# Performance work log

Measured on AMD Instinct MI355X. Metric: run time of the kernel, lower is better.

The kernel has to match this reference:

```python
import jax, jax.numpy as jnp
import numpy as np

EPS = 1e-5


def clin(xr, xi, Wr, Wi, br, bi):
    # complex linear layer: (xr + i xi) @ (Wr + i Wi) + (br + i bi)
    yr = xr @ Wr - xi @ Wi + br
    yi = xr @ Wi + xi @ Wr + bi
    return yr, yi


def setup_inputs() -> dict:
    key = jax.random.key(0)
    ks = jax.random.split(key, 16)
    B, N, DE, DV = 4, 256, 128, 64
    s_in = 1.0 / np.sqrt(DE)
    s_p = 1.0 / np.sqrt(DV)
    f32 = jnp.float32
    inp = {
        'Z_q': jax.random.normal(ks[0], (B, 2, N, DE), f32),
        'Z_k': jax.random.normal(ks[1], (B, 2, N, DE), f32),
        'Z_v': jax.random.normal(ks[2], (B, 2, N, DE), f32),
        't_measure_all': jnp.tile(jnp.arange(N + 1, dtype=f32) * 0.01, (B, 1)),
        'Wq_r': jax.random.normal(ks[3], (DE, DV), f32) * s_in,
        'Wq_i': jax.random.normal(ks[4], (DE, DV), f32) * s_in,
        'bq_r': jnp.zeros((DV,), f32), 'bq_i': jnp.zeros((DV,), f32),
        'Wk_r': jax.random.normal(ks[5], (DE, DV), f32) * s_in,
        'Wk_i': jax.random.normal(ks[6], (DE, DV), f32) * s_in,
        'bk_r': jnp.zeros((DV,), f32), 'bk_i': jnp.zeros((DV,), f32),
        'Wv_r': jax.random.normal(ks[7], (DE, DV), f32) * s_in,
        'Wv_i': jax.random.normal(ks[8], (DE, DV), f32) * s_in,
        'bv_r': jnp.zeros((DV,), f32), 'bv_i': jnp.zeros((DV,), f32),
        'Wp_r': jax.random.normal(ks[9], (DV, DE), f32) * s_p,
        'Wp_i': jax.random.normal(ks[10], (DV, DE), f32) * s_p,
        'bp_r': jnp.zeros((DE,), f32), 'bp_i': jnp.zeros((DE,), f32),
        'lambda1': jax.random.normal(ks[11], (2, DV // 2), f32),
        'lambda_Omega_sqrt': jax.random.normal(ks[12], (DV,), f32) / DV,
        'lambda_Gamma_sqrt': jax.random.normal(ks[13], (DV,), f32) / DV,
        'noise_floor': jnp.array(1.0, f32),
        'tau': jnp.array(1.0, f32),
        'nu': jnp.array(1.0, f32),
        'eta_param': jnp.zeros((DV,), f32),
    }
    return inp


def reference(Z_q, Z_k, Z_v, t_measure_all,
              Wq_r, Wq_i, bq_r, bq_i, Wk_r, Wk_i, bk_r, bk_i,
              Wv_r, Wv_i, bv_r, bv_i, Wp_r, Wp_i, bp_r, bp_i,
              lambda1, lambda_Omega_sqrt, lambda_Gamma_sqrt,
              noise_floor, tau, nu, eta_param):
    N = Z_q.shape[2]
    # complex projections (B, N, d)
    Qr, Qi = clin(Z_q[:, 0], Z_q[:, 1], Wq_r, Wq_i, bq_r, bq_i)
    Kr_, Ki_ = clin(Z_k[:, 0], Z_k[:, 1], Wk_r, Wk_i, bk_r, bk_i)
    Vr, Vi = clin(Z_v[:, 0], Z_v[:, 1], Wv_r, Wv_i, bv_r, bv_i)
    # state-transition eigenvalues: stable conjugate pairs
    re = jnp.concatenate([-lambda1[0] ** 2, -lambda1[0] ** 2])  # (d_v,), Re<=0
    im = jnp.concatenate([lambda1[1], -lambda1[1]])             # (d_v,)
    lam_Om = lambda_Omega_sqrt ** 2
    lam_Ga = lambda_Gamma_sqrt ** 2 + EPS
    # pairwise complex exponential kernel exp(lambda * (t_i - t_j))
    t = t_measure_all[0, :-1]                       # (N,)
    dt = t[:, None] - t[None, :]                    # (N, N)
    amp = jnp.exp(re[None, None, :] * dt[:, :, None])
    ph = im[None, None, :] * dt[:, :, None]
    Ker = amp * jnp.cos(ph)                          # (N, N, d_v)
    Kei = amp * jnp.sin(ph)
    # propagated value estimates Z_hat_ij = exp(lam dt_ij) * V_j
    Zhr = Ker[None] * Vr[:, None] - Kei[None] * Vi[:, None]  # (B, N, N, d_v)
    Zhi = Ker[None] * Vi[:, None] + Kei[None] * Vr[:, None]
    # residuals R_ij = Q_i - exp(lam dt_ij) * K_j
    Rr = Qr[:, :, None, :] - (Ker[None] * Kr_[:, None] - Kei[None] * Ki_[:, None])
    Ri = Qi[:, :, None, :] - (Ker[None] * Ki_[:, None] + Kei[None] * Kr_[:, None])
    # per-pair covariance (OU-process propagation of measurement + process noise)
    adt = jnp.abs(dt)[:, :, None]
    exp2 = jnp.exp(2.0 * re * adt)                   # (N, N, d_v)
    Vij = lam_Ga * exp2 + lam_Om * (exp2 - 1.0) / (2.0 * (re - EPS))
    # mahalanobis distance and attention scores
    mah = (Rr ** 2 + Ri ** 2) / (Vij[None] + lam_Ga)          # (B, N, N, d_v)
    dist_sum = jnp.abs(nu) * jnp.sum(mah, axis=3, keepdims=True)
    base = Vij[None] * (noise_floor + dist_sum + EPS)
    scores = -jnp.abs(tau) * jnp.log(base)
    mask = jnp.tril(jnp.ones((N, N), bool))
    scores = jnp.where(mask[None, :, :, None], scores, -jnp.inf)
    Qij = jax.nn.softmax(scores, axis=2)             # normalize over j
    m = mask[None, :, :, None].astype(Zhr.dtype)
    Zhr = Zhr * m
    Zhi = Zhi * m
    est_vr = jnp.einsum('bijd,bijd->bid', Qij, Zhr)
    est_vi = jnp.einsum('bijd,bijd->bid', Qij, Zhi)
    # gated residual mix (double sigmoid as in source)
    eta = jax.nn.sigmoid(eta_param)
    g = jax.nn.sigmoid(eta)
    elr = (1.0 - eta) * Vr + g * est_vr
    eli = (1.0 - eta) * Vi + g * est_vi
    # one-step-ahead prediction via matrix exponential exp(lambda * h)
    h = t[1] - t[0]
    ma = jnp.exp(re * h)
    mr, mi = ma * jnp.cos(im * h), ma * jnp.sin(im * h)
    ppr = mr * elr - mi * eli
    ppi = mr * eli + mi * elr
    outr, outi = clin(ppr, ppi, Wp_r, Wp_i, bp_r, bp_i)
    est_latent = jnp.stack([elr, eli], axis=1)       # (B, 2, N, d_v)
    out = jnp.stack([outr, outi], axis=1)            # (B, 2, N, d_e)
    Zhat = jnp.stack([Zhr, Zhi], axis=1)             # (B, 2, N, N, d_v)
    lambda_h = jnp.stack([re, im])                   # (2, d_v)
    return est_latent, out, Qij, Zhat, lambda_h
```

## Files before the change

### kernel.cpp

```cpp
#include <hip/hip_runtime.h>
#include <math.h>

#define B_ 4
#define N_ 256
#define DE_ 128
#define DV_ 64
#define EPS_ 1e-5f

typedef __attribute__((ext_vector_type(4))) float f32x4;

__device__ __forceinline__ f32x4 ld4(const float* p) { return *(const f32x4*)p; }
__device__ __forceinline__ void st4(float* p, f32x4 v) { *(f32x4*)p = v; }

#define OFF_ETA   0
#define OFF_G     64
#define OFF_MR    128
#define OFF_MI    192
#define OFF_KER   256
#define OFF_KEI   (OFF_KER + N_*DV_)
#define OFF_A     (OFF_KEI + N_*DV_)
#define OFF_INV   (OFF_A + N_*DV_)
#define OFF_QR    (OFF_INV + N_*DV_)
#define OFF_QI    (OFF_QR + B_*N_*DV_)
#define OFF_KR    (OFF_QI + B_*N_*DV_)
#define OFF_KI    (OFF_KR + B_*N_*DV_)
#define OFF_VR    (OFF_KI + B_*N_*DV_)
#define OFF_VI    (OFF_VR + B_*N_*DV_)

#define OUT_EL    0
#define OUT_OUT   (B_*2*N_*DV_)
#define OUT_QIJ   (OUT_OUT + B_*2*N_*DE_)
#define OUT_ZHAT  (OUT_QIJ + B_*N_*N_*DV_)
#define OUT_LAMH  (OUT_ZHAT + (size_t)B_*2*N_*N_*DV_)

__global__ __launch_bounds__(256) void k_pre(
    const float* __restrict__ Zq, const float* __restrict__ Zk, const float* __restrict__ Zv,
    const float* __restrict__ Wqr, const float* __restrict__ Wqi,
    const float* __restrict__ bqr, const float* __restrict__ bqi,
    const float* __restrict__ Wkr, const float* __restrict__ Wki,
    const float* __restrict__ bkr, const float* __restrict__ bki,
    const float* __restrict__ Wvr, const float* __restrict__ Wvi,
    const float* __restrict__ bvr, const float* __restrict__ bvi,
    const float* __restrict__ t,  const float* __restrict__ lam1,
    const float* __restrict__ lOm, const float* __restrict__ lGa,
    const float* __restrict__ eta_p, const float* __restrict__ tau_p,
    float* __restrict__ ws, float* __restrict__ out)
{
    const int tid = (int)threadIdx.x;

    if (blockIdx.x >= 1024) {
        const int idx = (int)blockIdx.x - 1024;
        const int w = tid >> 6;
        const int d = tid & 63;
        const int delta = idx * 4 + w;

        const float l0 = lam1[d & 31];
        const float re = -l0 * l0;
        const float im = (d < 32) ? lam1[32 + d] : -lam1[d];

        const float lo = lOm[d];
        const float lam_Om = lo * lo;
        const float lg_ = lGa[d];
        const float lam_Ga = lg_ * lg_ + EPS_;
        const float tau_a = fabsf(tau_p[0]);

        const float t0 = t[0];
        const float dt = t[delta] - t0;

        const float amp = expf(re * dt);
        const float ph  = im * dt;
        const int td = delta * DV_ + d;
        ws[OFF_KER + td] = amp * cosf(ph);
        ws[OFF_KEI + td] = amp * sinf(ph);

        const float e2  = expf(2.0f * re * dt);
        const float vij = lam_Ga * e2 + lam_Om * (e2 - 1.0f) / (2.0f * (re - EPS_));
        ws[OFF_A   + td] = expf(-tau_a * logf(vij));
        ws[OFF_INV + td] = 1.0f / (vij + lam_Ga);

        if (delta == 0) {
            const float eta = 1.0f / (1.0f + expf(-eta_p[d]));
            const float g   = 1.0f / (1.0f + expf(-eta));
            ws[OFF_ETA + d] = eta;
            ws[OFF_G   + d] = g;
            const float h  = t[1] - t0;
            const float ma = expf(re * h);
            ws[OFF_MR + d] = ma * cosf(im * h);
            ws[OFF_MI + d] = ma * sinf(im * h);
            out[OUT_LAMH + d]       = re;
            out[OUT_LAMH + DV_ + d] = im;
        }
        return;
    }

    const int row = (int)blockIdx.x;
    const int b = row >> 8, n = row & (N_ - 1);

    __shared__ float x[6][DE_];
    __shared__ float red[4][6][DV_];

    if (tid < DE_) {
        x[0][tid] = Zq[((size_t)(b*2+0)*N_ + n)*DE_ + tid];
        x[1][tid] = Zq[((size_t)(b*2+1)*N_ + n)*DE_ + tid];
        x[2][tid] = Zk[((size_t)(b*2+0)*N_ + n)*DE_ + tid];
        x[3][tid] = Zk[((size_t)(b*2+1)*N_ + n)*DE_ + tid];
        x[4][tid] = Zv[((size_t)(b*2+0)*N_ + n)*DE_ + tid];
        x[5][tid] = Zv[((size_t)(b*2+1)*N_ + n)*DE_ + tid];
    }
    __syncthreads();

    const int w = tid >> 6;
    const int d = tid & 63;
    float aqr = 0.f, aqi = 0.f, akr = 0.f, aki = 0.f, avr = 0.f, avi = 0.f;
    const int k0 = w * 32;
    #pragma unroll 4
    for (int kk = 0; kk < 32; ++kk) {
        const int k = k0 + kk;
        const float xqr = x[0][k], xqi = x[1][k];
        const float xkr = x[2][k], xki = x[3][k];
        const float xvr = x[4][k], xvi = x[5][k];
        float wr, wi;
        wr = Wqr[k*DV_ + d]; wi = Wqi[k*DV_ + d];
        aqr += xqr*wr - xqi*wi; aqi += xqr*wi + xqi*wr;
        wr = Wkr[k*DV_ + d]; wi = Wki[k*DV_ + d];
        akr += xkr*wr - xki*wi; aki += xkr*wi + xki*wr;
        wr = Wvr[k*DV_ + d]; wi = Wvi[k*DV_ + d];
        avr += xvr*wr - xvi*wi; avi += xvr*wi + xvi*wr;
    }
    red[w][0][d] = aqr; red[w][1][d] = aqi;
    red[w][2][d] = akr; red[w][3][d] = aki;
    red[w][4][d] = avr; red[w][5][d] = avi;
    __syncthreads();

    if (tid < DV_) {
        const int o = row * DV_ + tid;
        ws[OFF_QR + o] = red[0][0][tid]+red[1][0][tid]+red[2][0][tid]+red[3][0][tid] + bqr[tid];
        ws[OFF_QI + o] = red[0][1][tid]+red[1][1][tid]+red[2][1][tid]+red[3][1][tid] + bqi[tid];
        ws[OFF_KR + o] = red[0][2][tid]+red[1][2][tid]+red[2][2][tid]+red[3][2][tid] + bkr[tid];
        ws[OFF_KI + o] = red[0][3][tid]+red[1][3][tid]+red[2][3][tid]+red[3][3][tid] + bki[tid];
        ws[OFF_VR + o] = red[0][4][tid]+red[1][4][tid]+red[2][4][tid]+red[3][4][tid] + bvr[tid];
        ws[OFF_VI + o] = red[0][5][tid]+red[1][5][tid]+red[2][5][tid]+red[3][5][tid] + bvi[tid];
    }
}

__global__ __launch_bounds__(256) void k_main2(
    const float* __restrict__ ws, float* __restrict__ out,
    const float* __restrict__ Wpr, const float* __restrict__ Wpi,
    const float* __restrict__ bpr, const float* __restrict__ bpi,
    const float* __restrict__ nf_p, const float* __restrict__ tau_p,
    const float* __restrict__ nu_p)
{
    const int vb = (int)blockIdx.x;
    const int b = vb & 3;
    const int i = (N_ - 1) - (vb >> 2);
    const int row = b * N_ + i;
    const int tid = (int)threadIdx.x;
    const int wv = tid >> 6;
    const int l = tid & 63;
    const int g = l >> 4;
    const int q16 = l & 15;
    const int dq = q16 * 4;

    __shared__ float wl[N_];
    __shared__ f32x4 redS[4][16];
    __shared__ f32x4 redR[4][16];
    __shared__ f32x4 redI[4][16];
    __shared__ float ppr_s[DV_], ppi_s[DV_];

    const float nf    = nf_p[0];
    const float tau_a = fabsf(tau_p[0]);
    const float nu_a  = fabsf(nu_p[0]);

    const int nfull = (i + 1) >> 2;
    const int tail  = (i + 1) & 3;
    const f32x4 z4 = {0.f,0.f,0.f,0.f};

    float* qij = out + OUT_QIJ + (size_t)row * N_ * DV_;
    float* zro = out + OUT_ZHAT + ((size_t)(b*2+0)*N_ + i) * N_ * DV_;
    float* zio = out + OUT_ZHAT + ((size_t)(b*2+1)*N_ + i) * N_ * DV_;

    {
        const int jz0 = 4 * (nfull + (tail ? 1 : 0));
        const int nq = (N_ - jz0) * 16;
        for (int u = tid; u < nq; u += 256) {
            const int o = jz0*DV_ + u*4;
            st4(zro + o, z4);
            st4(zio + o, z4);
            st4(qij + o, z4);
        }
    }

    const f32x4 qr4 = ld4(ws + OFF_QR + row*DV_ + dq);
    const f32x4 qi4 = ld4(ws + OFF_QI + row*DV_ + dq);

    f32x4 s4  = {0.f,0.f,0.f,0.f};
    f32x4 evr = {0.f,0.f,0.f,0.f};
    f32x4 evi = {0.f,0.f,0.f,0.f};
    #pragma unroll 2
    for (int T = wv; T < nfull; T += 4) {
        const int j = 4*T + g;
        const int o = j*DV_ + dq;
        const int td = (i - j)*DV_ + dq;
        const f32x4 ker = ld4(ws + OFF_KER + td);
        const f32x4 kei = ld4(ws + OFF_KEI + td);
        const f32x4 vnv = ld4(ws + OFF_INV + td);
        const f32x4 a4  = ld4(ws + OFF_A   + td);
        const int kj = (b*N_ + j)*DV_ + dq;
        const f32x4 kr = ld4(ws + OFF_KR + kj);
        const f32x4 ki = ld4(ws + OFF_KI + kj);
        const f32x4 vr = ld4(ws + OFF_VR + kj);
        const f32x4 vi = ld4(ws + OFF_VI + kj);
        const f32x4 rr = qr4 - (ker*kr - kei*ki);
        const f32x4 ri = qi4 - (ker*ki + kei*kr);
        const f32x4 mah = (rr*rr + ri*ri) * vnv;
        float ds = mah[0] + mah[1] + mah[2] + mah[3];
        ds += __shfl_xor(ds, 1);
        ds += __shfl_xor(ds, 2);
        ds += __shfl_xor(ds, 4);
        ds += __shfl_xor(ds, 8);
        const float wj = expf(-tau_a * logf(nf + nu_a*ds + EPS_));
        if (q16 == 0) wl[j] = wj;
        const f32x4 zr = ker*vr - kei*vi;
        const f32x4 zi = ker*vi + kei*vr;
        st4(zro + o, zr);
        st4(zio + o, zi);
        const f32x4 qn = a4 * wj;
        s4  += qn;
        evr += qn * zr;
        evi += qn * zi;
    }
    if (tail && ((nfull & 3) == wv)) {
        const int j = 4*nfull + g;
        const int o = j*DV_ + dq;
        const bool act = (g < tail);
        const int td = (act ? (i - j) : 0)*DV_ + dq;
        const f32x4 ker = ld4(ws + OFF_KER + td);
        const f32x4 kei = ld4(ws + OFF_KEI + td);
        const f32x4 vnv = ld4(ws + OFF_INV + td);
        const f32x4 a4  = ld4(ws + OFF_A   + td);
        const int kj = (b*N_ + (act ? j : 0))*DV_ + dq;
        const f32x4 kr = ld4(ws + OFF_KR + kj);
        const f32x4 ki = ld4(ws + OFF_KI + kj);
        const f32x4 vr = ld4(ws + OFF_VR + kj);
        const f32x4 vi = ld4(ws + OFF_VI + kj);
        const f32x4 rr = qr4 - (ker*kr - kei*ki);
        const f32x4 ri = qi4 - (ker*ki + kei*kr);
        const f32x4 mah = (rr*rr + ri*ri) * vnv;
        float ds = mah[0] + mah[1] + mah[2] + mah[3];
        ds += __shfl_xor(ds, 1);
        ds += __shfl_xor(ds, 2);
        ds += __shfl_xor(ds, 4);
        ds += __shfl_xor(ds, 8);
        if (act) {
            const float wj = expf(-tau_a * logf(nf + nu_a*ds + EPS_));
            if (q16 == 0) wl[j] = wj;
            const f32x4 zr = ker*vr - kei*vi;
            const f32x4 zi = ker*vi + kei*vr;
            st4(zro + o, zr);
            st4(zio + o, zi);
            const f32x4 qn = a4 * wj;
            s4  += qn;
            evr += qn * zr;
            evi += qn * zi;
        } else {
            st4(zro + o, z4);
            st4(zio + o, z4);
        }
    }

    #pragma unroll
    for (int mask = 16; mask <= 32; mask <<= 1) {
        #pragma unroll
        for (int c = 0; c < 4; ++c) {
            s4[c]  += __shfl_xor(s4[c],  mask);
            evr[c] += __shfl_xor(evr[c], mask);
            evi[c] += __shfl_xor(evi[c], mask);
        }
    }
    if (g == 0) { redS[wv][q16] = s4; redR[wv][q16] = evr; redI[wv][q16] = evi; }
    __syncthreads();
    const f32x4 Z = redS[0][q16] + redS[1][q16] + redS[2][q16] + redS[3][q16];
    const f32x4 one = {1.f,1.f,1.f,1.f};
    const f32x4 invZ = one / Z;

    #pragma unroll 2
    for (int T = wv; T < nfull; T += 4) {
        const int j = 4*T + g;
        const int o = j*DV_ + dq;
        const int td = (i - j)*DV_ + dq;
        const f32x4 q4 = ld4(ws + OFF_A + td) * wl[j] * invZ;
        st4(qij + o, q4);
    }
    if (tail && ((nfull & 3) == wv)) {
        const int j = 4*nfull + g;
        const int o = j*DV_ + dq;
        if (g < tail) {
            const int td = (i - j)*DV_ + dq;
            const f32x4 q4 = ld4(ws + OFF_A + td) * wl[j] * invZ;
            st4(qij + o, q4);
        } else {
            st4(qij + o, z4);
        }
    }

    if (tid < 16) {
        const f32x4 Zt = redS[0][tid] + redS[1][tid] + redS[2][tid] + redS[3][tid];
        const f32x4 iZ = one / Zt;
        const f32x4 Evr = (redR[0][tid] + redR[1][tid] + redR[2][tid] + redR[3][tid]) * iZ;
        const f32x4 Evi = (redI[0][tid] + redI[1][tid] + redI[2][tid] + redI[3][tid]) * iZ;
        const int dq2 = tid * 4;
        const f32x4 vr  = ld4(ws + OFF_VR + row*DV_ + dq2);
        const f32x4 vi  = ld4(ws + OFF_VI + row*DV_ + dq2);
        const f32x4 eta = ld4(ws + OFF_ETA + dq2);
        const f32x4 gg  = ld4(ws + OFF_G + dq2);
        const f32x4 elr = (1.0f - eta)*vr + gg*Evr;
        const f32x4 eli = (1.0f - eta)*vi + gg*Evi;
        st4(out + OUT_EL + ((size_t)(b*2+0)*N_ + i)*DV_ + dq2, elr);
        st4(out + OUT_EL + ((size_t)(b*2+1)*N_ + i)*DV_ + dq2, eli);
        const f32x4 mr = ld4(ws + OFF_MR + dq2);
        const f32x4 mi = ld4(ws + OFF_MI + dq2);
        st4(ppr_s + dq2, mr*elr - mi*eli);
        st4(ppi_s + dq2, mr*eli + mi*elr);
    }
    __syncthreads();

    if (tid < DE_) {
        const int e = tid;
        float ar = bpr[e], ai = bpi[e];
        #pragma unroll 8
        for (int dd = 0; dd < DV_; ++dd) {
            const float wr = Wpr[dd*DE_ + e], wi = Wpi[dd*DE_ + e];
            const float r = ppr_s[dd], im = ppi_s[dd];
            ar += r*wr - im*wi;
            ai += r*wi + im*wr;
        }
        out[OUT_OUT + ((size_t)(b*2+0)*N_ + i)*DE_ + e] = ar;
        out[OUT_OUT + ((size_t)(b*2+1)*N_ + i)*DE_ + e] = ai;
    }
}

extern "C" void kernel_launch(void* const* d_in, const int* in_sizes, int n_in,
                              void* d_out, int out_size, void* d_ws, size_t ws_size,
                              hipStream_t stream)
{
    const float* Zq   = (const float*)d_in[0];
    const float* Zk   = (const float*)d_in[1];
    const float* Zv   = (const float*)d_in[2];
    const float* t    = (const float*)d_in[3];
    const float* Wqr  = (const float*)d_in[4];
    const float* Wqi  = (const float*)d_in[5];
    const float* bqr  = (const float*)d_in[6];
    const float* bqi  = (const float*)d_in[7];
    const float* Wkr  = (const float*)d_in[8];
    const float* Wki  = (const float*)d_in[9];
    const float* bkr  = (const float*)d_in[10];
    const float* bki  = (const float*)d_in[11];
    const float* Wvr  = (const float*)d_in[12];
    const float* Wvi  = (const float*)d_in[13];
    const float* bvr  = (const float*)d_in[14];
    const float* bvi  = (const float*)d_in[15];
    const float* Wpr  = (const float*)d_in[16];
    const float* Wpi  = (const float*)d_in[17];
    const float* bpr  = (const float*)d_in[18];
    const float* bpi  = (const float*)d_in[19];
    const float* lam1 = (const float*)d_in[20];
    const float* lOm  = (const float*)d_in[21];
    const float* lGa  = (const float*)d_in[22];
    const float* nf   = (const float*)d_in[23];
    const float* tau  = (const float*)d_in[24];
    const float* nu   = (const float*)d_in[25];
    const float* etap = (const float*)d_in[26];

    float* ws  = (float*)d_ws;
    float* out = (float*)d_out;

    k_pre<<<1024 + 64, 256, 0, stream>>>(Zq, Zk, Zv,
                                         Wqr, Wqi, bqr, bqi,
                                         Wkr, Wki, bkr, bki,
                                         Wvr, Wvi, bvr, bvi,
                                         t, lam1, lOm, lGa, etap, tau, ws, out);
    k_main2<<<B_*N_, 256, 0, stream>>>(ws, out, Wpr, Wpi, bpr, bpi, nf, tau, nu);
}
```

Before: 63.24 us.

## Move upper-triangle zero fill from main kernel into extra pre-kernel blocks

The zeroing of the masked (j > i) region of Zhat and Qij now happens in 1024 extra blocks of the projection kernel instead of inside each row block of the main kernel. Each fill block walks a fixed chunk of the output and stores zeros only where j > i. This evens out the work between rows, since the old per-row fill made low-i rows do nearly all the zero stores, and it lets the fill run alongside the projection work. The cost is extra index arithmetic and a branch for every element in the fill loop, including the lower-triangle elements that get skipped.

```diff
diff --git a/kernel.cpp b/kernel.cpp
--- a/kernel.cpp
+++ b/kernel.cpp
@@ -11,6 +11,12 @@
 
 __device__ __forceinline__ f32x4 ld4(const float* p) { return *(const f32x4*)p; }
 __device__ __forceinline__ void st4(float* p, f32x4 v) { *(f32x4*)p = v; }
+
+#define TQ_Z   8388608
+#define TQ_Q   4194304
+#define TQ_ALL (TQ_Z + TQ_Q)
+#define NFILL  1024
+#define CHUNK  (TQ_ALL / NFILL)
 
 #define OFF_ETA   0
 #define OFF_G     64
@@ -47,9 +53,30 @@
     float* __restrict__ ws, float* __restrict__ out)
 {
     const int tid = (int)threadIdx.x;
-
-    if (blockIdx.x >= 1024) {
-        const int idx = (int)blockIdx.x - 1024;
+    const int bid = (int)blockIdx.x;
+
+    if (bid >= 1088) {
+        const f32x4 z4 = {0.f,0.f,0.f,0.f};
+        const int fb = bid - 1088;
+        const int u0 = fb * CHUNK;
+        const int ue = u0 + CHUNK;
+        for (int u = u0 + tid; u < ue; u += 256) {
+            if (u < TQ_Z) {
+                const int j  = (u >> 4) & 255;
+                const int ii = (u >> 12) & 255;
+                if (j > ii) st4(out + OUT_ZHAT + (size_t)u*4, z4);
+            } else {
+                const int v  = u - TQ_Z;
+                const int j  = (v >> 4) & 255;
+                const int ii = (v >> 12) & 255;
+                if (j > ii) st4(out + OUT_QIJ + (size_t)v*4, z4);
+            }
+        }
+        return;
+    }
+
+    if (bid >= 1024) {
+        const int idx = bid - 1024;
         const int w = tid >> 6;
         const int d = tid & 63;
         const int delta = idx * 4 + w;
@@ -93,7 +120,7 @@
         return;
     }
 
-    const int row = (int)blockIdx.x;
+    const int row = bid;
     const int b = row >> 8, n = row & (N_ - 1);
 
     __shared__ float x[6][DE_];
@@ -173,22 +200,10 @@
 
     const int nfull = (i + 1) >> 2;
     const int tail  = (i + 1) & 3;
-    const f32x4 z4 = {0.f,0.f,0.f,0.f};
 
     float* qij = out + OUT_QIJ + (size_t)row * N_ * DV_;
     float* zro = out + OUT_ZHAT + ((size_t)(b*2+0)*N_ + i) * N_ * DV_;
     float* zio = out + OUT_ZHAT + ((size_t)(b*2+1)*N_ + i) * N_ * DV_;
-
-    {
-        const int jz0 = 4 * (nfull + (tail ? 1 : 0));
-        const int nq = (N_ - jz0) * 16;
-        for (int u = tid; u < nq; u += 256) {
-            const int o = jz0*DV_ + u*4;
-            st4(zro + o, z4);
-            st4(zio + o, z4);
-            st4(qij + o, z4);
-        }
-    }
 
     const f32x4 qr4 = ld4(ws + OFF_QR + row*DV_ + dq);
     const f32x4 qi4 = ld4(ws + OFF_QI + row*DV_ + dq);
@@ -262,9 +277,6 @@
             s4  += qn;
             evr += qn * zr;
             evi += qn * zi;
-        } else {
-            st4(zro + o, z4);
-            st4(zio + o, z4);
         }
     }
 
@@ -291,16 +303,12 @@
         const f32x4 q4 = ld4(ws + OFF_A + td) * wl[j] * invZ;
         st4(qij + o, q4);
     }
-    if (tail && ((nfull & 3) == wv)) {
+    if (tail && ((nfull & 3) == wv) && (g < tail)) {
         const int j = 4*nfull + g;
         const int o = j*DV_ + dq;
-        if (g < tail) {
-            const int td = (i - j)*DV_ + dq;
-            const f32x4 q4 = ld4(ws + OFF_A + td) * wl[j] * invZ;
-            st4(qij + o, q4);
-        } else {
-            st4(qij + o, z4);
-        }
+        const int td = (i - j)*DV_ + dq;
+        const f32x4 q4 = ld4(ws + OFF_A + td) * wl[j] * invZ;
+        st4(qij + o, q4);
     }
 
     if (tid < 16) {
@@ -374,10 +382,10 @@
     float* ws  = (float*)d_ws;
     float* out = (float*)d_out;
 
-    k_pre<<<1024 + 64, 256, 0, stream>>>(Zq, Zk, Zv,
-                                         Wqr, Wqi, bqr, bqi,
-                                         Wkr, Wki, bkr, bki,
-                                         Wvr, Wvi, bvr, bvi,
-                                         t, lam1, lOm, lGa, etap, tau, ws, out);
+    k_pre<<<1024 + 64 + NFILL, 256, 0, stream>>>(Zq, Zk, Zv,
+                                                 Wqr, Wqi, bqr, bqi,
+                                                 Wkr, Wki, bkr, bki,
+                                                 Wvr, Wvi, bvr, bvi,
+                                                 t, lam1, lOm, lGa, etap, tau, ws, out);
     k_main2<<<B_*N_, 256, 0, stream>>>(ws, out, Wpr, Wpi, bpr, bpi, nf, tau, nu);
 }
```

New measurement: 66.76 us. 1.06x slower.
